# Kernel optimization log

Hardware: AMD Instinct MI355X
Metric: run time of the kernel (lower is better)

## Reference

```python
import jax, jax.numpy as jnp
import numpy as np

GROUPS = 16
EPS_GN = 1e-6
EPS_L2 = 1e-12


def setup_inputs() -> dict:
    key = jax.random.key(0)
    ks = jax.random.split(key, 5)
    B, C, H, W = 8, 256, 64, 64
    s = 0.02
    return {
        "x": jax.random.normal(ks[0], (B, C, H, W), dtype=jnp.float32),
        "gn_gamma": jnp.ones((C,), dtype=jnp.float32),
        "gn_beta": jnp.zeros((C,), dtype=jnp.float32),
        "qkv_w": jax.random.normal(ks[1], (3 * C, C), dtype=jnp.float32) * s,
        "qkv_b": jax.random.normal(ks[2], (3 * C,), dtype=jnp.float32) * s,
        "temperature": jnp.ones((1, 1, 1), dtype=jnp.float32),  # (num_heads,1,1)
        "proj_w": jax.random.normal(ks[3], (C, C), dtype=jnp.float32) * s,
        "proj_b": jax.random.normal(ks[4], (C,), dtype=jnp.float32) * s,
    }


def _group_norm(x, gamma, beta):
    B, C, H, W = x.shape
    xg = x.reshape(B, GROUPS, C // GROUPS, H, W)
    mu = xg.mean(axis=(2, 3, 4), keepdims=True)
    var = xg.var(axis=(2, 3, 4), keepdims=True)
    xn = ((xg - mu) * jax.lax.rsqrt(var + EPS_GN)).reshape(B, C, H, W)
    return xn * gamma[None, :, None, None] + beta[None, :, None, None]


def _l2norm(t):
    # normalize along last axis (token axis N), matching F.normalize eps semantics
    n = jnp.sqrt(jnp.sum(t * t, axis=-1, keepdims=True))
    return t / jnp.maximum(n, EPS_L2)


def reference(x, gn_gamma, gn_beta, qkv_w, qkv_b, temperature, proj_w, proj_b):
    B, C, H, W = x.shape
    N = H * W
    nh = 1
    dh = C // nh

    h = _group_norm(x, gn_gamma, gn_beta).reshape(B, C, N).transpose(0, 2, 1)  # (B,N,C)

    qkv = h @ qkv_w.T + qkv_b                                   # (B,N,3C)
    qkv = qkv.reshape(B, N, 3, nh, dh).transpose(2, 0, 3, 4, 1)  # (3,B,nh,dh,N)
    q, k, v = qkv[0], qkv[1], qkv[2]

    q = _l2norm(q)
    k = _l2norm(k)

    # channel cross-covariance attention: (B,nh,dh,dh)
    attn = jax.nn.softmax(jnp.einsum('bhcn,bhdn->bhcd', q, k) * temperature[None], axis=-1)
    out = jnp.einsum('bhcd,bhdn->bhcn', attn, v)                 # (B,nh,dh,N)
    out = out.transpose(0, 3, 1, 2).reshape(B, N, C)             # (B,N,C)
    out = out @ proj_w.T + proj_b

    return x + out.transpose(0, 2, 1).reshape(B, C, H, W)
```

## Files before the change

### kernel.cpp

```cpp
#include <hip/hip_runtime.h>
#include <hip/hip_bf16.h>

namespace {

constexpr float EPS_GN = 1e-6f;
constexpr float EPS_L2 = 1e-12f;

typedef __attribute__((ext_vector_type(8))) short bf16x8;
typedef __attribute__((ext_vector_type(4))) float f32x4;

__device__ __forceinline__ unsigned short f2bf(float f) {
  union { __hip_bfloat16 h; unsigned short u; } cv;
  cv.h = __float2bfloat16(f);
  return cv.u;
}
__device__ __forceinline__ float blo(unsigned u) { return __uint_as_float(u << 16); }
__device__ __forceinline__ float bhi(unsigned u) { return __uint_as_float(u & 0xffff0000u); }

__global__ __launch_bounds__(256) void prep_k(const float* __restrict__ x,
                                              const float* __restrict__ qkv_w,
                                              const float* __restrict__ proj_w,
                                              unsigned short* __restrict__ xbf,
                                              unsigned short* __restrict__ xT,
                                              float* __restrict__ sxpart,
                                              unsigned short* __restrict__ qkvw_bf,
                                              unsigned short* __restrict__ pw_bf,
                                              unsigned short* __restrict__ wvt_bf) {
  __shared__ char shm[16640];
  const int bid = blockIdx.x, t = threadIdx.x;
  if (bid < 2048) {
    unsigned short (*tl)[68] = (unsigned short (*)[68])shm;
    const int b = bid >> 8, cy = (bid >> 6) & 3, nx = bid & 63;
    const int c0 = cy * 64, n0 = nx * 64;
    const int cl = t >> 2, ns = (t & 3) * 16;
    const float* xp = x + ((size_t)b << 20) + (size_t)(c0 + cl) * 4096 + n0 + ns;
    unsigned pk[8];
    float s = 0.f;
#pragma unroll
    for (int q = 0; q < 4; ++q) {
      float4 v = *(const float4*)(xp + q * 4);
      s += v.x + v.y + v.z + v.w;
      pk[2 * q + 0] = f2bf(v.x) | ((unsigned)f2bf(v.y) << 16);
      pk[2 * q + 1] = f2bf(v.z) | ((unsigned)f2bf(v.w) << 16);
    }
    unsigned short* xo = xbf + ((size_t)b << 20) + (size_t)(c0 + cl) * 4096 + n0 + ns;
    *(int4*)xo = make_int4((int)pk[0], (int)pk[1], (int)pk[2], (int)pk[3]);
    *(int4*)(xo + 8) = make_int4((int)pk[4], (int)pk[5], (int)pk[6], (int)pk[7]);
#pragma unroll
    for (int q = 0; q < 8; ++q)
      *(unsigned*)(&tl[cl][ns + 2 * q]) = pk[q];
    s += __shfl_xor(s, 1);
    s += __shfl_xor(s, 2);
    if ((t & 3) == 0)
      sxpart[((size_t)((b * 4 + cy) * 64 + cl)) * 64 + nx] = s;
    __syncthreads();
    const int nl = t >> 2, cs2 = (t & 3) * 16;
    unsigned pk2[8];
#pragma unroll
    for (int q = 0; q < 8; ++q)
      pk2[q] = (unsigned)(unsigned short)tl[cs2 + 2 * q][nl] |
               ((unsigned)(unsigned short)tl[cs2 + 2 * q + 1][nl] << 16);
    unsigned short* to = xT + ((size_t)((b << 12) + n0 + nl)) * 256 + c0 + cs2;
    *(int4*)to = make_int4((int)pk2[0], (int)pk2[1], (int)pk2[2], (int)pk2[3]);
    *(int4*)(to + 8) = make_int4((int)pk2[4], (int)pk2[5], (int)pk2[6], (int)pk2[7]);
    return;
  }
  const int cb = bid - 2048;
  if (cb < 256) {
    const float* src = (cb < 192) ? qkv_w : proj_w;
    unsigned short* dst = (cb < 192) ? qkvw_bf : pw_bf;
    int i = (cb < 192 ? cb : cb - 192) * 256 + t;
    float4 v = ((const float4*)src)[i];
    unsigned p0 = f2bf(v.x) | ((unsigned)f2bf(v.y) << 16);
    unsigned p1 = f2bf(v.z) | ((unsigned)f2bf(v.w) << 16);
    ((int2*)dst)[i] = make_int2((int)p0, (int)p1);
    return;
  }
  float (*tlf)[65] = (float (*)[65])shm;
  const int tb = cb - 256;
  const int j0 = (tb >> 2) * 64, d0 = (tb & 3) * 64;
  const float* src = qkv_w + 512 * 256;
  const int jr = t >> 2, ds = (t & 3) * 16;
#pragma unroll
  for (int q = 0; q < 4; ++q) {
    float4 v = *(const float4*)(src + (size_t)(j0 + jr) * 256 + d0 + ds + q * 4);
    tlf[jr][ds + q * 4 + 0] = v.x; tlf[jr][ds + q * 4 + 1] = v.y;
    tlf[jr][ds + q * 4 + 2] = v.z; tlf[jr][ds + q * 4 + 3] = v.w;
  }
  __syncthreads();
  const int dr = t >> 2, js = (t & 3) * 16;
  unsigned pk[8];
#pragma unroll
  for (int q = 0; q < 8; ++q)
    pk[q] = f2bf(tlf[js + 2 * q][dr]) | ((unsigned)f2bf(tlf[js + 2 * q + 1][dr]) << 16);
  unsigned short* dp = wvt_bf + (size_t)(d0 + dr) * 256 + j0 + js;
  *(int4*)dp = make_int4((int)pk[0], (int)pk[1], (int)pk[2], (int)pk[3]);
  *(int4*)(dp + 8) = make_int4((int)pk[4], (int)pk[5], (int)pk[6], (int)pk[7]);
}

#define NT64_BODY(APTR, ALDA, BPTR, BLDB, KSTEPS)                                   \
  const int tid = threadIdx.x;                                                      \
  const int l = tid & 63, w = tid >> 6;                                             \
  const int wm = w >> 1, wn = w & 1;                                                \
  const int r = tid >> 2;                                                           \
  const unsigned short* aG = (APTR) + (size_t)(m0 + r) * (ALDA) + (tid & 3) * 16;   \
  const unsigned short* bG = (BPTR) + (size_t)(n0 + r) * (BLDB) + (tid & 3) * 16;   \
  const int g0 = (tid & 3) * 2;                                                     \
  const int w0 = r * 128 + (((g0)     ^ (r & 7)) << 4);                             \
  const int w1 = r * 128 + (((g0 + 1) ^ (r & 7)) << 4);                             \
  int rdA[2], rdB[2];                                                               \
  _Pragma("unroll")                                                                 \
  for (int i = 0; i < 2; ++i) {                                                     \
    int rm = wm * 32 + i * 16 + (l & 15);                                           \
    rdA[i] = rm * 128 + (((l >> 4) ^ (rm & 7)) << 4);                               \
    int rn = wn * 32 + i * 16 + (l & 15);                                           \
    rdB[i] = rn * 128 + (((l >> 4) ^ (rn & 7)) << 4);                               \
  }                                                                                 \
  f32x4 zero = {0.f, 0.f, 0.f, 0.f};                                                \
  f32x4 acc[2][2] = {{zero, zero}, {zero, zero}};                                   \
  for (int ks = 0; ks < (KSTEPS); ++ks) {                                           \
    int4 a0 = *(const int4*)aG, a1 = *(const int4*)(aG + 8);                        \
    int4 b0 = *(const int4*)bG, b1 = *(const int4*)(bG + 8);                        \
    aG += 64; bG += 64;                                                             \
    __syncthreads();                                                                \
    *(int4*)((char*)As + w0) = a0; *(int4*)((char*)As + w1) = a1;                   \
    *(int4*)((char*)Bs + w0) = b0; *(int4*)((char*)Bs + w1) = b1;                   \
    __syncthreads();                                                                \
    _Pragma("unroll")                                                               \
    for (int kk = 0; kk < 2; ++kk) {                                                \
      bf16x8 af[2], bf_[2];                                                         \
      _Pragma("unroll")                                                             \
      for (int i = 0; i < 2; ++i) {                                                 \
        af[i]  = *(const bf16x8*)((const char*)As + (rdA[i] ^ (kk << 6)));          \
        bf_[i] = *(const bf16x8*)((const char*)Bs + (rdB[i] ^ (kk << 6)));          \
      }                                                                             \
      _Pragma("unroll")                                                             \
      for (int i = 0; i < 2; ++i)                                                   \
        _Pragma("unroll")                                                           \
        for (int j = 0; j < 2; ++j)                                                 \
          acc[i][j] = __builtin_amdgcn_mfma_f32_16x16x32_bf16(af[i], bf_[j],        \
                                                              acc[i][j], 0, 0, 0); \
    }                                                                               \
  }                                                                                 \
  const int mB = m0 + wm * 32 + ((l >> 4) << 2);                                    \
  const int nB = n0 + wn * 32 + (l & 15);

__global__ __launch_bounds__(256) void sxx64_k(const unsigned short* __restrict__ xbf,
                                               float* __restrict__ part) {
  __shared__ unsigned short As[4096];
  __shared__ unsigned short Bs[4096];
  const int z = blockIdx.z;
  const int b = z >> 3, sl = z & 7;
  const int m0 = blockIdx.y << 6, n0 = blockIdx.x << 6;
  const unsigned short* base = xbf + ((size_t)b << 20) + (size_t)sl * 512;
  NT64_BODY(base, 4096, base, 4096, 8)
  float* po = part + ((size_t)z << 16);
#pragma unroll
  for (int i = 0; i < 2; ++i)
#pragma unroll
    for (int rr = 0; rr < 4; ++rr)
#pragma unroll
      for (int j = 0; j < 2; ++j)
        po[(size_t)(mB + i * 16 + rr) * 256 + nB + j * 16] = acc[i][j][rr];
}

__global__ __launch_bounds__(256) void out64_k(const unsigned short* __restrict__ Fbf,
                                               const unsigned short* __restrict__ xT,
                                               const float* __restrict__ hvec,
                                               float* __restrict__ outF) {
  __shared__ unsigned short As[4096];
  __shared__ unsigned short Bs[4096];
  const int b = blockIdx.z;
  const int m0 = blockIdx.y << 6, n0 = blockIdx.x << 6;
  NT64_BODY(Fbf + ((size_t)b << 16), 256, xT + ((size_t)b << 20), 256, 4)
#pragma unroll
  for (int i = 0; i < 2; ++i) {
#pragma unroll
    for (int rr = 0; rr < 4; ++rr) {
      int mi = mB + i * 16 + rr;
      float hv = hvec[b * 256 + mi];
      size_t rowo = ((size_t)b << 20) + (size_t)mi * 4096;
#pragma unroll
      for (int j = 0; j < 2; ++j)
        outF[rowo + nB + j * 16] = acc[i][j][rr] + hv;
    }
  }
}

__global__ __launch_bounds__(256) void ugemm_k(const unsigned short* __restrict__ qkvw,
                                               const unsigned short* __restrict__ Gbf,
                                               unsigned short* __restrict__ Ubf) {
  __shared__ unsigned short As[4096];
  __shared__ unsigned short Bs[4096];
  const int b = blockIdx.z;
  const int m0 = blockIdx.y << 6, n0 = blockIdx.x << 6;
  NT64_BODY(qkvw, 256, Gbf + ((size_t)b << 16), 256, 4)
  unsigned short* pu = Ubf + ((size_t)b << 17);
#pragma unroll
  for (int i = 0; i < 2; ++i)
#pragma unroll
    for (int rr = 0; rr < 4; ++rr)
#pragma unroll
      for (int j = 0; j < 2; ++j)
        pu[(size_t)(mB + i * 16 + rr) * 256 + nB + j * 16] = f2bf(acc[i][j][rr]);
}

__global__ __launch_bounds__(256) void y1h_k(const unsigned short* __restrict__ wvt,
                                             const unsigned short* __restrict__ Abf,
                                             const float* __restrict__ abv,
                                             const float* __restrict__ proj_w,
                                             const float* __restrict__ proj_b,
                                             unsigned short* __restrict__ Y1,
                                             float* __restrict__ hvec) {
  __shared__ unsigned short As[4096];
  __shared__ unsigned short Bs[4096];
  __shared__ float abl[256];
  const int b = blockIdx.z;
  const int m0 = blockIdx.y << 6, n0 = blockIdx.x << 6;
  NT64_BODY(wvt, 256, Abf + ((size_t)b << 16), 256, 4)
  unsigned short* pu = Y1 + ((size_t)b << 16);
#pragma unroll
  for (int i = 0; i < 2; ++i)
#pragma unroll
    for (int rr = 0; rr < 4; ++rr)
#pragma unroll
      for (int j = 0; j < 2; ++j)
        pu[(size_t)(mB + i * 16 + rr) * 256 + nB + j * 16] = f2bf(acc[i][j][rr]);
  if (blockIdx.y == 0) {
    abl[tid] = abv[b * 256 + tid];
    __syncthreads();
    const int t = n0 + (tid >> 2);
    const int qd = (tid & 3) * 64;
    const float* pr = proj_w + (size_t)t * 256 + qd;
    float s = 0.f;
#pragma unroll 8
    for (int i = 0; i < 64; ++i) s += pr[i] * abl[qd + i];
    s += __shfl_xor(s, 1);
    s += __shfl_xor(s, 2);
    if ((tid & 3) == 0) hvec[b * 256 + t] = proj_b[t] + s;
  }
}

__global__ __launch_bounds__(256) void fgen_k(const unsigned short* __restrict__ pw,
                                              const unsigned short* __restrict__ Y1,
                                              const float* __restrict__ avec,
                                              const float* __restrict__ evec,
                                              unsigned short* __restrict__ Fbf,
                                              float* __restrict__ hvec) {
  __shared__ unsigned short As[4096];
  __shared__ unsigned short Bs[4096];
  const int b = blockIdx.z;
  const int m0 = blockIdx.y << 6, n0 = blockIdx.x << 6;
  NT64_BODY(pw, 256, Y1 + ((size_t)b << 16), 256, 4)
  __syncthreads();
  float* hred = (float*)As;
  if (tid < 64) hred[tid] = 0.f;
  __syncthreads();
#pragma unroll
  for (int i = 0; i < 2; ++i) {
#pragma unroll
    for (int rr = 0; rr < 4; ++rr) {
      int t = mB + i * 16 + rr;
      float hp = 0.f;
#pragma unroll
      for (int j = 0; j < 2; ++j) {
        int d = nB + j * 16;
        float f = acc[i][j][rr];
        float fa = f * avec[b * 256 + d] + (t == d ? 1.f : 0.f);
        Fbf[((size_t)b << 16) + (size_t)t * 256 + d] = f2bf(fa);
        hp += f * evec[b * 256 + d];
      }
      atomicAdd(&hred[t - m0], hp);
    }
  }
  __syncthreads();
  if (tid < 64) atomicAdd(&hvec[b * 256 + m0 + tid], hred[tid]);
}

__global__ __launch_bounds__(256) void stats_k(
    const float* __restrict__ part, const float* __restrict__ sxpart,
    const float* __restrict__ gamma, const float* __restrict__ beta,
    const unsigned short* __restrict__ qkvw_bf,
    float* __restrict__ avec, float* __restrict__ evec,
    float* __restrict__ sxvec, float* __restrict__ wsv) {
  const int b = blockIdx.x, c = threadIdx.x;
  const float* sp = sxpart + ((size_t)(b * 256 + c) << 6);
  float sxv = 0.f;
#pragma unroll 4
  for (int t = 0; t < 64; ++t) sxv += sp[t];
  float dg = 0.f;
#pragma unroll
  for (int s = 0; s < 8; ++s) dg += part[((size_t)(b * 8 + s) << 16) + c * 257];
  float gs = sxv, g2 = dg;
#pragma unroll
  for (int off = 1; off < 16; off <<= 1) {
    gs += __shfl_xor(gs, off);
    g2 += __shfl_xor(g2, off);
  }
  const float inv = 1.f / 65536.f;
  float mu = gs * inv;
  float var = g2 * inv - mu * mu;
  float rstd = rsqrtf(var + EPS_GN);
  float av = gamma[c] * rstd;
  float ev = beta[c] - mu * av;
  float sv = av * sxv + 4096.f * ev;
  avec[b * 256 + c] = av; evec[b * 256 + c] = ev;
  sxvec[b * 256 + c] = sxv;
  __shared__ float sl_[256];
  sl_[c] = sv;
  __syncthreads();
  for (int i = c; i < 512; i += 256) {
    const unsigned short* wr = qkvw_bf + (size_t)i * 256;
    float acc = 0.f;
    for (int d = 0; d < 256; d += 8) {
      int4 v = *(const int4*)(wr + d);
      acc += blo((unsigned)v.x) * sl_[d + 0] + bhi((unsigned)v.x) * sl_[d + 1];
      acc += blo((unsigned)v.y) * sl_[d + 2] + bhi((unsigned)v.y) * sl_[d + 3];
      acc += blo((unsigned)v.z) * sl_[d + 4] + bhi((unsigned)v.z) * sl_[d + 5];
      acc += blo((unsigned)v.w) * sl_[d + 6] + bhi((unsigned)v.w) * sl_[d + 7];
    }
    wsv[b * 512 + i] = acc;
  }
}

__global__ __launch_bounds__(256) void gfill_k(const float* __restrict__ part,
                                               const float* __restrict__ avec,
                                               const float* __restrict__ evec,
                                               const float* __restrict__ sxvec,
                                               unsigned short* __restrict__ Gbf) {
  const int b = blockIdx.y;
  const int r = blockIdx.x * 16 + (threadIdx.x >> 4);
  const int cs = (threadIdx.x & 15) * 16;
  const float ac = avec[b * 256 + r], ec = evec[b * 256 + r], sxc = sxvec[b * 256 + r];
  unsigned pk[8];
#pragma unroll
  for (int q = 0; q < 8; ++q) {
    unsigned lohi[2];
#pragma unroll
    for (int h = 0; h < 2; ++h) {
      int d = cs + 2 * q + h;
      float S = 0.f;
#pragma unroll
      for (int s = 0; s < 8; ++s)
        S += part[(((size_t)(b * 8 + s)) << 16) + (size_t)r * 256 + d];
      float ad = avec[b * 256 + d], ed = evec[b * 256 + d], sxd = sxvec[b * 256 + d];
      float gv = ac * ad * S + ac * ed * sxc + ec * ad * sxd + 4096.f * ec * ed;
      lohi[h] = f2bf(gv);
    }
    pk[q] = lohi[0] | (lohi[1] << 16);
  }
  unsigned short* gp = Gbf + ((size_t)b << 16) + (size_t)r * 256 + cs;
  *(int4*)gp = make_int4((int)pk[0], (int)pk[1], (int)pk[2], (int)pk[3]);
  *(int4*)(gp + 8) = make_int4((int)pk[4], (int)pk[5], (int)pk[6], (int)pk[7]);
}

__global__ __launch_bounds__(256) void logsm_k(
    const unsigned short* __restrict__ Ubf,
    const unsigned short* __restrict__ qkvw,
    const float* __restrict__ wsv,
    const float* __restrict__ qkv_b, const float* __restrict__ temp,
    unsigned short* __restrict__ Abf, float* __restrict__ abv) {
  __shared__ unsigned short As[64 * 64];
  __shared__ unsigned short Bs[256 * 64];
  const int b = blockIdx.y, m0 = blockIdx.x * 64;
  const int tid = threadIdx.x;
  const int l = tid & 63, w = tid >> 6;
  const unsigned short* wk = qkvw + 65536;

  const int ar = tid >> 2, ac = tid & 3;
  const unsigned short* aG = Ubf + ((size_t)b << 17) + (size_t)(m0 + ar) * 256 + ac * 16;
  const unsigned short* bG = wk + (size_t)tid * 256;
  const int g0 = ac * 2;
  const int wA0 = ar * 128 + (((g0)     ^ (ar & 7)) << 4);
  const int wA1 = ar * 128 + (((g0 + 1) ^ (ar & 7)) << 4);
  int wBoff[8];
#pragma unroll
  for (int c = 0; c < 8; ++c) wBoff[c] = tid * 128 + ((c ^ (tid & 7)) << 4);

  int rdA;
  { int rm = w * 16 + (l & 15); rdA = rm * 128 + (((l >> 4) ^ (rm & 7)) << 4); }
  int rdB[16];
#pragma unroll
  for (int nf = 0; nf < 16; ++nf) {
    int rn = nf * 16 + (l & 15);
    rdB[nf] = rn * 128 + (((l >> 4) ^ (rn & 7)) << 4);
  }

  f32x4 zero = {0.f, 0.f, 0.f, 0.f};
  f32x4 acc[16];
#pragma unroll
  for (int nf = 0; nf < 16; ++nf) acc[nf] = zero;

  for (int ks = 0; ks < 4; ++ks) {
    int4 a0 = *(const int4*)aG;
    int4 a1 = *(const int4*)(aG + 8);
    int4 bv[8];
#pragma unroll
    for (int c = 0; c < 8; ++c) bv[c] = *(const int4*)(bG + c * 8);
    aG += 64; bG += 64;
    __syncthreads();
    *(int4*)((char*)As + wA0) = a0;
    *(int4*)((char*)As + wA1) = a1;
#pragma unroll
    for (int c = 0; c < 8; ++c) *(int4*)((char*)Bs + wBoff[c]) = bv[c];
    __syncthreads();
#pragma unroll
    for (int kk = 0; kk < 2; ++kk) {
      bf16x8 af = *(const bf16x8*)((const char*)As + (rdA ^ (kk << 6)));
#pragma unroll
      for (int nf = 0; nf < 16; ++nf) {
        bf16x8 bf_ = *(const bf16x8*)((const char*)Bs + (rdB[nf] ^ (kk << 6)));
        acc[nf] = __builtin_amdgcn_mfma_f32_16x16x32_bf16(af, bf_, acc[nf], 0, 0, 0);
      }
    }
  }

  __syncthreads();
  float* sKs  = (float*)As;
  float* sWks = sKs + 256;
  float* sBk  = sWks + 256;
  float* sBv  = sBk + 256;
  float* sQs  = sBv + 256;
  {
    const unsigned short* ur = Ubf + ((size_t)b << 17) + (size_t)(256 + tid) * 256;
    const unsigned short* wr = wk + (size_t)tid * 256;
    float dot = 0.f;
    for (int dd = 0; dd < 256; dd += 8) {
      int4 uv = *(const int4*)(ur + dd);
      int4 wv = *(const int4*)(wr + dd);
      dot += blo((unsigned)uv.x) * blo((unsigned)wv.x) + bhi((unsigned)uv.x) * bhi((unsigned)wv.x);
      dot += blo((unsigned)uv.y) * blo((unsigned)wv.y) + bhi((unsigned)uv.y) * bhi((unsigned)wv.y);
      dot += blo((unsigned)uv.z) * blo((unsigned)wv.z) + bhi((unsigned)uv.z) * bhi((unsigned)wv.z);
      dot += blo((unsigned)uv.w) * blo((unsigned)wv.w) + bhi((unsigned)uv.w) * bhi((unsigned)wv.w);
    }
    float bk = qkv_b[256 + tid];
    float wks = wsv[b * 512 + 256 + tid];
    float n2 = dot + 2.f * bk * wks + 4096.f * bk * bk;
    sKs[tid]  = 1.f / fmaxf(sqrtf(fmaxf(n2, 0.f)), EPS_L2);
    sWks[tid] = wks;
    sBk[tid]  = bk;
    sBv[tid]  = qkv_b[512 + tid];
  }
  if (tid < 64) {
    int m = m0 + tid;
    const unsigned short* ur = Ubf + ((size_t)b << 17) + (size_t)m * 256;
    const unsigned short* wr = qkvw + (size_t)m * 256;
    float dot = 0.f;
    for (int dd = 0; dd < 256; dd += 8) {
      int4 uv = *(const int4*)(ur + dd);
      int4 wv = *(const int4*)(wr + dd);
      dot += blo((unsigned)uv.x) * blo((unsigned)wv.x) + bhi((unsigned)uv.x) * bhi((unsigned)wv.x);
      dot += blo((unsigned)uv.y) * blo((unsigned)wv.y) + bhi((unsigned)uv.y) * bhi((unsigned)wv.y);
      dot += blo((unsigned)uv.z) * blo((unsigned)wv.z) + bhi((unsigned)uv.z) * bhi((unsigned)wv.z);
      dot += blo((unsigned)uv.w) * blo((unsigned)wv.w) + bhi((unsigned)uv.w) * bhi((unsigned)wv.w);
    }
    float bq = qkv_b[m], wqs = wsv[b * 512 + m];
    float n2 = dot + 2.f * bq * wqs + 4096.f * bq * bq;
    sQs[tid] = 1.f / fmaxf(sqrtf(fmaxf(n2, 0.f)), EPS_L2);
  }
  __syncthreads();

  const float T = temp[0];
  const int lrow = w * 16 + ((l >> 4) << 2);
  const int mrow = m0 + lrow;
  float ks_c[16], wks_c[16], bk_c[16], bv_c[16];
#pragma unroll
  for (int nf = 0; nf < 16; ++nf) {
    int n = nf * 16 + (l & 15);
    ks_c[nf] = sKs[n]; wks_c[nf] = sWks[n]; bk_c[nf] = sBk[n]; bv_c[nf] = sBv[n];
  }
#pragma unroll
  for (int rr = 0; rr < 4; ++rr) {
    int m = mrow + rr;
    float qs = sQs[lrow + rr], wqs = wsv[b * 512 + m], bq = qkv_b[m];
    float sc = T * qs;
#pragma unroll
    for (int nf = 0; nf < 16; ++nf)
      acc[nf][rr] = sc * ks_c[nf] *
                    (acc[nf][rr] + bq * wks_c[nf] + bk_c[nf] * wqs + 4096.f * bq * bk_c[nf]);
    float mx = acc[0][rr];
#pragma unroll
    for (int nf = 1; nf < 16; ++nf) mx = fmaxf(mx, acc[nf][rr]);
    mx = fmaxf(mx, __shfl_xor(mx, 1));
    mx = fmaxf(mx, __shfl_xor(mx, 2));
    mx = fmaxf(mx, __shfl_xor(mx, 4));
    mx = fmaxf(mx, __shfl_xor(mx, 8));
    float s = 0.f, ab = 0.f;
#pragma unroll
    for (int nf = 0; nf < 16; ++nf) {
      float e = __expf(acc[nf][rr] - mx);
      acc[nf][rr] = e;
      s += e; ab += e * bv_c[nf];
    }
#pragma unroll
    for (int off = 1; off < 16; off <<= 1) {
      s += __shfl_xor(s, off);
      ab += __shfl_xor(ab, off);
    }
    float inv = 1.f / s;
    unsigned short* arow = Abf + ((size_t)b << 16) + (size_t)m * 256 + (l & 15);
#pragma unroll
    for (int nf = 0; nf < 16; ++nf)
      arow[nf * 16] = f2bf(acc[nf][rr] * inv);
    if ((l & 15) == 0) abv[b * 256 + m] = ab * inv;
  }
}

}

extern "C" void kernel_launch(void* const* d_in, const int* in_sizes, int n_in,
                              void* d_out, int out_size, void* d_ws, size_t ws_size,
                              hipStream_t stream) {
  const float* x      = (const float*)d_in[0];
  const float* gamma  = (const float*)d_in[1];
  const float* beta   = (const float*)d_in[2];
  const float* qkv_w  = (const float*)d_in[3];
  const float* qkv_b  = (const float*)d_in[4];
  const float* temp   = (const float*)d_in[5];
  const float* proj_w = (const float*)d_in[6];
  const float* proj_b = (const float*)d_in[7];
  float* out = (float*)d_out;

  char* ws = (char*)d_ws;
  const size_t MB = 1048576;
  unsigned short* qkvw_bf = (unsigned short*)(ws);
  unsigned short* pw_bf   = (unsigned short*)(ws + 0x60000);
  unsigned short* wvt_bf  = (unsigned short*)(ws + 0x80000);
  float* avec  = (float*)(ws + 0xA0000);
  float* evec  = (float*)(ws + 0xA2000);
  float* sxvec = (float*)(ws + 0xA4000);
  float* wsv   = (float*)(ws + 0xA6000);
  float* hvec  = (float*)(ws + 0xAA000);
  float* abv   = (float*)(ws + 0xAC000);
  float* sxpart = (float*)(ws + 1 * MB);
  float* part   = (float*)(ws + 2 * MB);
  unsigned short* Gbf = (unsigned short*)(ws + 18 * MB);
  unsigned short* Ubf = (unsigned short*)(ws + 19 * MB);
  unsigned short* Abf = (unsigned short*)(ws + 21 * MB);
  unsigned short* Y1  = (unsigned short*)(ws + 22 * MB);
  unsigned short* Fbf = (unsigned short*)(ws + 23 * MB);
  unsigned short* xbf = (unsigned short*)(ws + 24 * MB);
  unsigned short* xT  = (unsigned short*)(ws + 40 * MB);
  if (ws_size < 56 * MB) return;

  prep_k<<<2320, 256, 0, stream>>>(x, qkv_w, proj_w, xbf, xT, sxpart,
                                   qkvw_bf, pw_bf, wvt_bf);

  sxx64_k<<<dim3(4, 4, 64), 256, 0, stream>>>(xbf, part);

  stats_k<<<8, 256, 0, stream>>>(part, sxpart, gamma, beta, qkvw_bf,
                                 avec, evec, sxvec, wsv);

  gfill_k<<<dim3(16, 8), 256, 0, stream>>>(part, avec, evec, sxvec, Gbf);

  ugemm_k<<<dim3(4, 8, 8), 256, 0, stream>>>(qkvw_bf, Gbf, Ubf);

  logsm_k<<<dim3(4, 8), 256, 0, stream>>>(Ubf, qkvw_bf, wsv, qkv_b, temp, Abf, abv);

  y1h_k<<<dim3(4, 4, 8), 256, 0, stream>>>(wvt_bf, Abf, abv, proj_w, proj_b, Y1, hvec);

  fgen_k<<<dim3(4, 4, 8), 256, 0, stream>>>(pw_bf, Y1, avec, evec, Fbf, hvec);

  out64_k<<<dim3(64, 4, 8), 256, 0, stream>>>(Fbf, xT, hvec, out);
}
```

Measured before the change: 115.9 us.

## Fuse six small mid-pipeline kernels into one cooperative kernel with grid syncs

Replaces the stats, gfill, ugemm, logsm, y1h and fgen launches with a single cooperative kernel of 256 blocks that runs each stage in turn, separated by grid-wide barriers. The aim is to remove the launch overhead and inter-kernel gaps between these tiny, low-occupancy stages. In exchange, most blocks sit idle in several stages, and each grid sync has its own cost. It also depends on all 256 blocks being co-resident.

```diff
diff --git a/kernel.cpp b/kernel.cpp
--- a/kernel.cpp
+++ b/kernel.cpp
@@ -1,5 +1,8 @@
 #include <hip/hip_runtime.h>
 #include <hip/hip_bf16.h>
+#include <hip/hip_cooperative_groups.h>
+
+namespace cg = cooperative_groups;
 
 namespace {
 
@@ -187,322 +190,319 @@
   }
 }
 
-__global__ __launch_bounds__(256) void ugemm_k(const unsigned short* __restrict__ qkvw,
-                                               const unsigned short* __restrict__ Gbf,
-                                               unsigned short* __restrict__ Ubf) {
-  __shared__ unsigned short As[4096];
-  __shared__ unsigned short Bs[4096];
-  const int b = blockIdx.z;
-  const int m0 = blockIdx.y << 6, n0 = blockIdx.x << 6;
-  NT64_BODY(qkvw, 256, Gbf + ((size_t)b << 16), 256, 4)
-  unsigned short* pu = Ubf + ((size_t)b << 17);
-#pragma unroll
-  for (int i = 0; i < 2; ++i)
-#pragma unroll
-    for (int rr = 0; rr < 4; ++rr)
-#pragma unroll
-      for (int j = 0; j < 2; ++j)
-        pu[(size_t)(mB + i * 16 + rr) * 256 + nB + j * 16] = f2bf(acc[i][j][rr]);
-}
-
-__global__ __launch_bounds__(256) void y1h_k(const unsigned short* __restrict__ wvt,
-                                             const unsigned short* __restrict__ Abf,
-                                             const float* __restrict__ abv,
-                                             const float* __restrict__ proj_w,
-                                             const float* __restrict__ proj_b,
-                                             unsigned short* __restrict__ Y1,
-                                             float* __restrict__ hvec) {
-  __shared__ unsigned short As[4096];
-  __shared__ unsigned short Bs[4096];
-  __shared__ float abl[256];
-  const int b = blockIdx.z;
-  const int m0 = blockIdx.y << 6, n0 = blockIdx.x << 6;
-  NT64_BODY(wvt, 256, Abf + ((size_t)b << 16), 256, 4)
-  unsigned short* pu = Y1 + ((size_t)b << 16);
-#pragma unroll
-  for (int i = 0; i < 2; ++i)
-#pragma unroll
-    for (int rr = 0; rr < 4; ++rr)
-#pragma unroll
-      for (int j = 0; j < 2; ++j)
-        pu[(size_t)(mB + i * 16 + rr) * 256 + nB + j * 16] = f2bf(acc[i][j][rr]);
-  if (blockIdx.y == 0) {
-    abl[tid] = abv[b * 256 + tid];
-    __syncthreads();
-    const int t = n0 + (tid >> 2);
-    const int qd = (tid & 3) * 64;
-    const float* pr = proj_w + (size_t)t * 256 + qd;
-    float s = 0.f;
+struct MidArgs {
+  const float* part; const float* sxpart;
+  const float* gamma; const float* beta;
+  const unsigned short* qkvw; const unsigned short* wvt; const unsigned short* pw;
+  const float* qkv_b; const float* temp;
+  const float* proj_w; const float* proj_b;
+  float* avec; float* evec; float* sxvec; float* wsv;
+  unsigned short* Gbf; unsigned short* Ubf; unsigned short* Abf;
+  unsigned short* Y1; unsigned short* Fbf;
+  float* abv; float* hvec;
+};
+
+__global__ __launch_bounds__(256) void mid_k(MidArgs p) {
+  __shared__ char shm[40960];
+  cg::grid_group gridg = cg::this_grid();
+  const int blk = blockIdx.x;
+
+  if (blk < 8) {
+    const int b = blk, c = threadIdx.x;
+    const float* sp = p.sxpart + ((size_t)(b * 256 + c) << 6);
+    float sxv = 0.f;
+#pragma unroll 4
+    for (int t = 0; t < 64; ++t) sxv += sp[t];
+    float dg = 0.f;
+#pragma unroll
+    for (int s = 0; s < 8; ++s) dg += p.part[((size_t)(b * 8 + s) << 16) + c * 257];
+    float gs = sxv, g2 = dg;
+#pragma unroll
+    for (int off = 1; off < 16; off <<= 1) {
+      gs += __shfl_xor(gs, off);
+      g2 += __shfl_xor(g2, off);
+    }
+    const float inv = 1.f / 65536.f;
+    float mu = gs * inv;
+    float var = g2 * inv - mu * mu;
+    float rstd = rsqrtf(var + EPS_GN);
+    float av = p.gamma[c] * rstd;
+    float ev = p.beta[c] - mu * av;
+    float sv = av * sxv + 4096.f * ev;
+    p.avec[b * 256 + c] = av; p.evec[b * 256 + c] = ev;
+    p.sxvec[b * 256 + c] = sxv;
+    float* sl_ = (float*)shm;
+    sl_[c] = sv;
+    __syncthreads();
+    for (int i = c; i < 512; i += 256) {
+      const unsigned short* wr = p.qkvw + (size_t)i * 256;
+      float acc = 0.f;
+      for (int d = 0; d < 256; d += 8) {
+        int4 v = *(const int4*)(wr + d);
+        acc += blo((unsigned)v.x) * sl_[d + 0] + bhi((unsigned)v.x) * sl_[d + 1];
+        acc += blo((unsigned)v.y) * sl_[d + 2] + bhi((unsigned)v.y) * sl_[d + 3];
+        acc += blo((unsigned)v.z) * sl_[d + 4] + bhi((unsigned)v.z) * sl_[d + 5];
+        acc += blo((unsigned)v.w) * sl_[d + 6] + bhi((unsigned)v.w) * sl_[d + 7];
+      }
+      p.wsv[b * 512 + i] = acc;
+    }
+  }
+  gridg.sync();
+
+  if (blk < 128) {
+    const int b = blk >> 4;
+    const int r = (blk & 15) * 16 + (threadIdx.x >> 4);
+    const int cs = (threadIdx.x & 15) * 16;
+    const float ac = p.avec[b * 256 + r], ec = p.evec[b * 256 + r], sxc = p.sxvec[b * 256 + r];
+    unsigned pk[8];
+#pragma unroll
+    for (int q = 0; q < 8; ++q) {
+      unsigned lohi[2];
+#pragma unroll
+      for (int h = 0; h < 2; ++h) {
+        int d = cs + 2 * q + h;
+        float S = 0.f;
+#pragma unroll
+        for (int s = 0; s < 8; ++s)
+          S += p.part[(((size_t)(b * 8 + s)) << 16) + (size_t)r * 256 + d];
+        float ad = p.avec[b * 256 + d], ed = p.evec[b * 256 + d], sxd = p.sxvec[b * 256 + d];
+        float gv = ac * ad * S + ac * ed * sxc + ec * ad * sxd + 4096.f * ec * ed;
+        lohi[h] = f2bf(gv);
+      }
+      pk[q] = lohi[0] | (lohi[1] << 16);
+    }
+    unsigned short* gp = p.Gbf + ((size_t)b << 16) + (size_t)r * 256 + cs;
+    *(int4*)gp = make_int4((int)pk[0], (int)pk[1], (int)pk[2], (int)pk[3]);
+    *(int4*)(gp + 8) = make_int4((int)pk[4], (int)pk[5], (int)pk[6], (int)pk[7]);
+  }
+  gridg.sync();
+
+  {
+    const int b = blk >> 5;
+    const int m0 = ((blk >> 2) & 7) << 6, n0 = (blk & 3) << 6;
+    unsigned short* As = (unsigned short*)shm;
+    unsigned short* Bs = (unsigned short*)(shm + 8192);
+    NT64_BODY(p.qkvw, 256, p.Gbf + ((size_t)b << 16), 256, 4)
+    unsigned short* pu = p.Ubf + ((size_t)b << 17);
+#pragma unroll
+    for (int i = 0; i < 2; ++i)
+#pragma unroll
+      for (int rr = 0; rr < 4; ++rr)
+#pragma unroll
+        for (int j = 0; j < 2; ++j)
+          pu[(size_t)(mB + i * 16 + rr) * 256 + nB + j * 16] = f2bf(acc[i][j][rr]);
+  }
+  gridg.sync();
+
+  if (blk < 32) {
+    const int b = blk >> 2, m0 = (blk & 3) * 64;
+    const int tid = threadIdx.x;
+    const int l = tid & 63, w = tid >> 6;
+    unsigned short* As = (unsigned short*)shm;
+    unsigned short* Bs = (unsigned short*)(shm + 8192);
+    const unsigned short* wk = p.qkvw + 65536;
+
+    const int ar = tid >> 2, ac = tid & 3;
+    const unsigned short* aG = p.Ubf + ((size_t)b << 17) + (size_t)(m0 + ar) * 256 + ac * 16;
+    const unsigned short* bG = wk + (size_t)tid * 256;
+    const int g0 = ac * 2;
+    const int wA0 = ar * 128 + (((g0)     ^ (ar & 7)) << 4);
+    const int wA1 = ar * 128 + (((g0 + 1) ^ (ar & 7)) << 4);
+    int wBoff[8];
+#pragma unroll
+    for (int c = 0; c < 8; ++c) wBoff[c] = tid * 128 + ((c ^ (tid & 7)) << 4);
+
+    int rdA;
+    { int rm = w * 16 + (l & 15); rdA = rm * 128 + (((l >> 4) ^ (rm & 7)) << 4); }
+    int rdB[16];
+#pragma unroll
+    for (int nf = 0; nf < 16; ++nf) {
+      int rn = nf * 16 + (l & 15);
+      rdB[nf] = rn * 128 + (((l >> 4) ^ (rn & 7)) << 4);
+    }
+
+    f32x4 zero = {0.f, 0.f, 0.f, 0.f};
+    f32x4 acc[16];
+#pragma unroll
+    for (int nf = 0; nf < 16; ++nf) acc[nf] = zero;
+
+    for (int ks = 0; ks < 4; ++ks) {
+      int4 a0 = *(const int4*)aG;
+      int4 a1 = *(const int4*)(aG + 8);
+      int4 bv[8];
+#pragma unroll
+      for (int c = 0; c < 8; ++c) bv[c] = *(const int4*)(bG + c * 8);
+      aG += 64; bG += 64;
+      __syncthreads();
+      *(int4*)((char*)As + wA0) = a0;
+      *(int4*)((char*)As + wA1) = a1;
+#pragma unroll
+      for (int c = 0; c < 8; ++c) *(int4*)((char*)Bs + wBoff[c]) = bv[c];
+      __syncthreads();
+#pragma unroll
+      for (int kk = 0; kk < 2; ++kk) {
+        bf16x8 af = *(const bf16x8*)((const char*)As + (rdA ^ (kk << 6)));
+#pragma unroll
+        for (int nf = 0; nf < 16; ++nf) {
+          bf16x8 bf_ = *(const bf16x8*)((const char*)Bs + (rdB[nf] ^ (kk << 6)));
+          acc[nf] = __builtin_amdgcn_mfma_f32_16x16x32_bf16(af, bf_, acc[nf], 0, 0, 0);
+        }
+      }
+    }
+
+    __syncthreads();
+    float* sKs  = (float*)As;
+    float* sWks = sKs + 256;
+    float* sBk  = sWks + 256;
+    float* sBv  = sBk + 256;
+    float* sQs  = sBv + 256;
+    {
+      const unsigned short* ur = p.Ubf + ((size_t)b << 17) + (size_t)(256 + tid) * 256;
+      const unsigned short* wr = wk + (size_t)tid * 256;
+      float dot = 0.f;
+      for (int dd = 0; dd < 256; dd += 8) {
+        int4 uv = *(const int4*)(ur + dd);
+        int4 wv = *(const int4*)(wr + dd);
+        dot += blo((unsigned)uv.x) * blo((unsigned)wv.x) + bhi((unsigned)uv.x) * bhi((unsigned)wv.x);
+        dot += blo((unsigned)uv.y) * blo((unsigned)wv.y) + bhi((unsigned)uv.y) * bhi((unsigned)wv.y);
+        dot += blo((unsigned)uv.z) * blo((unsigned)wv.z) + bhi((unsigned)uv.z) * bhi((unsigned)wv.z);
+        dot += blo((unsigned)uv.w) * blo((unsigned)wv.w) + bhi((unsigned)uv.w) * bhi((unsigned)wv.w);
+      }
+      float bk = p.qkv_b[256 + tid];
+      float wks = p.wsv[b * 512 + 256 + tid];
+      float n2 = dot + 2.f * bk * wks + 4096.f * bk * bk;
+      sKs[tid]  = 1.f / fmaxf(sqrtf(fmaxf(n2, 0.f)), EPS_L2);
+      sWks[tid] = wks;
+      sBk[tid]  = bk;
+      sBv[tid]  = p.qkv_b[512 + tid];
+    }
+    if (tid < 64) {
+      int m = m0 + tid;
+      const unsigned short* ur = p.Ubf + ((size_t)b << 17) + (size_t)m * 256;
+      const unsigned short* wr = p.qkvw + (size_t)m * 256;
+      float dot = 0.f;
+      for (int dd = 0; dd < 256; dd += 8) {
+        int4 uv = *(const int4*)(ur + dd);
+        int4 wv = *(const int4*)(wr + dd);
+        dot += blo((unsigned)uv.x) * blo((unsigned)wv.x) + bhi((unsigned)uv.x) * bhi((unsigned)wv.x);
+        dot += blo((unsigned)uv.y) * blo((unsigned)wv.y) + bhi((unsigned)uv.y) * bhi((unsigned)wv.y);
+        dot += blo((unsigned)uv.z) * blo((unsigned)wv.z) + bhi((unsigned)uv.z) * bhi((unsigned)wv.z);
+        dot += blo((unsigned)uv.w) * blo((unsigned)wv.w) + bhi((unsigned)uv.w) * bhi((unsigned)wv.w);
+      }
+      float bq = p.qkv_b[m], wqs = p.wsv[b * 512 + m];
+      float n2 = dot + 2.f * bq * wqs + 4096.f * bq * bq;
+      sQs[tid] = 1.f / fmaxf(sqrtf(fmaxf(n2, 0.f)), EPS_L2);
+    }
+    __syncthreads();
+
+    const float T = p.temp[0];
+    const int lrow = w * 16 + ((l >> 4) << 2);
+    const int mrow = m0 + lrow;
+    float ks_c[16], wks_c[16], bk_c[16], bv_c[16];
+#pragma unroll
+    for (int nf = 0; nf < 16; ++nf) {
+      int n = nf * 16 + (l & 15);
+      ks_c[nf] = sKs[n]; wks_c[nf] = sWks[n]; bk_c[nf] = sBk[n]; bv_c[nf] = sBv[n];
+    }
+#pragma unroll
+    for (int rr = 0; rr < 4; ++rr) {
+      int m = mrow + rr;
+      float qs = sQs[lrow + rr], wqs = p.wsv[b * 512 + m], bq = p.qkv_b[m];
+      float sc = T * qs;
+#pragma unroll
+      for (int nf = 0; nf < 16; ++nf)
+        acc[nf][rr] = sc * ks_c[nf] *
+                      (acc[nf][rr] + bq * wks_c[nf] + bk_c[nf] * wqs + 4096.f * bq * bk_c[nf]);
+      float mx = acc[0][rr];
+#pragma unroll
+      for (int nf = 1; nf < 16; ++nf) mx = fmaxf(mx, acc[nf][rr]);
+      mx = fmaxf(mx, __shfl_xor(mx, 1));
+      mx = fmaxf(mx, __shfl_xor(mx, 2));
+      mx = fmaxf(mx, __shfl_xor(mx, 4));
+      mx = fmaxf(mx, __shfl_xor(mx, 8));
+      float s = 0.f, ab = 0.f;
+#pragma unroll
+      for (int nf = 0; nf < 16; ++nf) {
+        float e = __expf(acc[nf][rr] - mx);
+        acc[nf][rr] = e;
+        s += e; ab += e * bv_c[nf];
+      }
+#pragma unroll
+      for (int off = 1; off < 16; off <<= 1) {
+        s += __shfl_xor(s, off);
+        ab += __shfl_xor(ab, off);
+      }
+      float inv = 1.f / s;
+      unsigned short* arow = p.Abf + ((size_t)b << 16) + (size_t)m * 256 + (l & 15);
+#pragma unroll
+      for (int nf = 0; nf < 16; ++nf)
+        arow[nf * 16] = f2bf(acc[nf][rr] * inv);
+      if ((l & 15) == 0) p.abv[b * 256 + m] = ab * inv;
+    }
+  }
+  gridg.sync();
+
+  if (blk < 128) {
+    const int b = blk >> 4;
+    const int by = (blk >> 2) & 3;
+    const int m0 = by << 6, n0 = (blk & 3) << 6;
+    unsigned short* As = (unsigned short*)shm;
+    unsigned short* Bs = (unsigned short*)(shm + 8192);
+    float* abl = (float*)(shm + 16384);
+    NT64_BODY(p.wvt, 256, p.Abf + ((size_t)b << 16), 256, 4)
+    unsigned short* pu = p.Y1 + ((size_t)b << 16);
+#pragma unroll
+    for (int i = 0; i < 2; ++i)
+#pragma unroll
+      for (int rr = 0; rr < 4; ++rr)
+#pragma unroll
+        for (int j = 0; j < 2; ++j)
+          pu[(size_t)(mB + i * 16 + rr) * 256 + nB + j * 16] = f2bf(acc[i][j][rr]);
+    if (by == 0) {
+      abl[tid] = p.abv[b * 256 + tid];
+      __syncthreads();
+      const int t = n0 + (tid >> 2);
+      const int qd = (tid & 3) * 64;
+      const float* pr = p.proj_w + (size_t)t * 256 + qd;
+      float s = 0.f;
 #pragma unroll 8
-    for (int i = 0; i < 64; ++i) s += pr[i] * abl[qd + i];
-    s += __shfl_xor(s, 1);
-    s += __shfl_xor(s, 2);
-    if ((tid & 3) == 0) hvec[b * 256 + t] = proj_b[t] + s;
-  }
-}
-
-__global__ __launch_bounds__(256) void fgen_k(const unsigned short* __restrict__ pw,
-                                              const unsigned short* __restrict__ Y1,
-                                              const float* __restrict__ avec,
-                                              const float* __restrict__ evec,
-                                              unsigned short* __restrict__ Fbf,
-                                              float* __restrict__ hvec) {
-  __shared__ unsigned short As[4096];
-  __shared__ unsigned short Bs[4096];
-  const int b = blockIdx.z;
-  const int m0 = blockIdx.y << 6, n0 = blockIdx.x << 6;
-  NT64_BODY(pw, 256, Y1 + ((size_t)b << 16), 256, 4)
-  __syncthreads();
-  float* hred = (float*)As;
-  if (tid < 64) hred[tid] = 0.f;
-  __syncthreads();
-#pragma unroll
-  for (int i = 0; i < 2; ++i) {
-#pragma unroll
-    for (int rr = 0; rr < 4; ++rr) {
-      int t = mB + i * 16 + rr;
-      float hp = 0.f;
-#pragma unroll
-      for (int j = 0; j < 2; ++j) {
-        int d = nB + j * 16;
-        float f = acc[i][j][rr];
-        float fa = f * avec[b * 256 + d] + (t == d ? 1.f : 0.f);
-        Fbf[((size_t)b << 16) + (size_t)t * 256 + d] = f2bf(fa);
-        hp += f * evec[b * 256 + d];
-      }
-      atomicAdd(&hred[t - m0], hp);
-    }
-  }
-  __syncthreads();
-  if (tid < 64) atomicAdd(&hvec[b * 256 + m0 + tid], hred[tid]);
-}
-
-__global__ __launch_bounds__(256) void stats_k(
-    const float* __restrict__ part, const float* __restrict__ sxpart,
-    const float* __restrict__ gamma, const float* __restrict__ beta,
-    const unsigned short* __restrict__ qkvw_bf,
-    float* __restrict__ avec, float* __restrict__ evec,
-    float* __restrict__ sxvec, float* __restrict__ wsv) {
-  const int b = blockIdx.x, c = threadIdx.x;
-  const float* sp = sxpart + ((size_t)(b * 256 + c) << 6);
-  float sxv = 0.f;
-#pragma unroll 4
-  for (int t = 0; t < 64; ++t) sxv += sp[t];
-  float dg = 0.f;
-#pragma unroll
-  for (int s = 0; s < 8; ++s) dg += part[((size_t)(b * 8 + s) << 16) + c * 257];
-  float gs = sxv, g2 = dg;
-#pragma unroll
-  for (int off = 1; off < 16; off <<= 1) {
-    gs += __shfl_xor(gs, off);
-    g2 += __shfl_xor(g2, off);
-  }
-  const float inv = 1.f / 65536.f;
-  float mu = gs * inv;
-  float var = g2 * inv - mu * mu;
-  float rstd = rsqrtf(var + EPS_GN);
-  float av = gamma[c] * rstd;
-  float ev = beta[c] - mu * av;
-  float sv = av * sxv + 4096.f * ev;
-  avec[b * 256 + c] = av; evec[b * 256 + c] = ev;
-  sxvec[b * 256 + c] = sxv;
-  __shared__ float sl_[256];
-  sl_[c] = sv;
-  __syncthreads();
-  for (int i = c; i < 512; i += 256) {
-    const unsigned short* wr = qkvw_bf + (size_t)i * 256;
-    float acc = 0.f;
-    for (int d = 0; d < 256; d += 8) {
-      int4 v = *(const int4*)(wr + d);
-      acc += blo((unsigned)v.x) * sl_[d + 0] + bhi((unsigned)v.x) * sl_[d + 1];
-      acc += blo((unsigned)v.y) * sl_[d + 2] + bhi((unsigned)v.y) * sl_[d + 3];
-      acc += blo((unsigned)v.z) * sl_[d + 4] + bhi((unsigned)v.z) * sl_[d + 5];
-      acc += blo((unsigned)v.w) * sl_[d + 6] + bhi((unsigned)v.w) * sl_[d + 7];
-    }
-    wsv[b * 512 + i] = acc;
-  }
-}
-
-__global__ __launch_bounds__(256) void gfill_k(const float* __restrict__ part,
-                                               const float* __restrict__ avec,
-                                               const float* __restrict__ evec,
-                                               const float* __restrict__ sxvec,
-                                               unsigned short* __restrict__ Gbf) {
-  const int b = blockIdx.y;
-  const int r = blockIdx.x * 16 + (threadIdx.x >> 4);
-  const int cs = (threadIdx.x & 15) * 16;
-  const float ac = avec[b * 256 + r], ec = evec[b * 256 + r], sxc = sxvec[b * 256 + r];
-  unsigned pk[8];
-#pragma unroll
-  for (int q = 0; q < 8; ++q) {
-    unsigned lohi[2];
-#pragma unroll
-    for (int h = 0; h < 2; ++h) {
-      int d = cs + 2 * q + h;
-      float S = 0.f;
-#pragma unroll
-      for (int s = 0; s < 8; ++s)
-        S += part[(((size_t)(b * 8 + s)) << 16) + (size_t)r * 256 + d];
-      float ad = avec[b * 256 + d], ed = evec[b * 256 + d], sxd = sxvec[b * 256 + d];
-      float gv = ac * ad * S + ac * ed * sxc + ec * ad * sxd + 4096.f * ec * ed;
-      lohi[h] = f2bf(gv);
-    }
-    pk[q] = lohi[0] | (lohi[1] << 16);
-  }
-  unsigned short* gp = Gbf + ((size_t)b << 16) + (size_t)r * 256 + cs;
-  *(int4*)gp = make_int4((int)pk[0], (int)pk[1], (int)pk[2], (int)pk[3]);
-  *(int4*)(gp + 8) = make_int4((int)pk[4], (int)pk[5], (int)pk[6], (int)pk[7]);
-}
-
-__global__ __launch_bounds__(256) void logsm_k(
-    const unsigned short* __restrict__ Ubf,
-    const unsigned short* __restrict__ qkvw,
-    const float* __restrict__ wsv,
-    const float* __restrict__ qkv_b, const float* __restrict__ temp,
-    unsigned short* __restrict__ Abf, float* __restrict__ abv) {
-  __shared__ unsigned short As[64 * 64];
-  __shared__ unsigned short Bs[256 * 64];
-  const int b = blockIdx.y, m0 = blockIdx.x * 64;
-  const int tid = threadIdx.x;
-  const int l = tid & 63, w = tid >> 6;
-  const unsigned short* wk = qkvw + 65536;
-
-  const int ar = tid >> 2, ac = tid & 3;
-  const unsigned short* aG = Ubf + ((size_t)b << 17) + (size_t)(m0 + ar) * 256 + ac * 16;
-  const unsigned short* bG = wk + (size_t)tid * 256;
-  const int g0 = ac * 2;
-  const int wA0 = ar * 128 + (((g0)     ^ (ar & 7)) << 4);
-  const int wA1 = ar * 128 + (((g0 + 1) ^ (ar & 7)) << 4);
-  int wBoff[8];
-#pragma unroll
-  for (int c = 0; c < 8; ++c) wBoff[c] = tid * 128 + ((c ^ (tid & 7)) << 4);
-
-  int rdA;
-  { int rm = w * 16 + (l & 15); rdA = rm * 128 + (((l >> 4) ^ (rm & 7)) << 4); }
-  int rdB[16];
-#pragma unroll
-  for (int nf = 0; nf < 16; ++nf) {
-    int rn = nf * 16 + (l & 15);
-    rdB[nf] = rn * 128 + (((l >> 4) ^ (rn & 7)) << 4);
-  }
-
-  f32x4 zero = {0.f, 0.f, 0.f, 0.f};
-  f32x4 acc[16];
-#pragma unroll
-  for (int nf = 0; nf < 16; ++nf) acc[nf] = zero;
-
-  for (int ks = 0; ks < 4; ++ks) {
-    int4 a0 = *(const int4*)aG;
-    int4 a1 = *(const int4*)(aG + 8);
-    int4 bv[8];
-#pragma unroll
-    for (int c = 0; c < 8; ++c) bv[c] = *(const int4*)(bG + c * 8);
-    aG += 64; bG += 64;
-    __syncthreads();
-    *(int4*)((char*)As + wA0) = a0;
-    *(int4*)((char*)As + wA1) = a1;
-#pragma unroll
-    for (int c = 0; c < 8; ++c) *(int4*)((char*)Bs + wBoff[c]) = bv[c];
-    __syncthreads();
-#pragma unroll
-    for (int kk = 0; kk < 2; ++kk) {
-      bf16x8 af = *(const bf16x8*)((const char*)As + (rdA ^ (kk << 6)));
-#pragma unroll
-      for (int nf = 0; nf < 16; ++nf) {
-        bf16x8 bf_ = *(const bf16x8*)((const char*)Bs + (rdB[nf] ^ (kk << 6)));
-        acc[nf] = __builtin_amdgcn_mfma_f32_16x16x32_bf16(af, bf_, acc[nf], 0, 0, 0);
-      }
-    }
-  }
-
-  __syncthreads();
-  float* sKs  = (float*)As;
-  float* sWks = sKs + 256;
-  float* sBk  = sWks + 256;
-  float* sBv  = sBk + 256;
-  float* sQs  = sBv + 256;
-  {
-    const unsigned short* ur = Ubf + ((size_t)b << 17) + (size_t)(256 + tid) * 256;
-    const unsigned short* wr = wk + (size_t)tid * 256;
-    float dot = 0.f;
-    for (int dd = 0; dd < 256; dd += 8) {
-      int4 uv = *(const int4*)(ur + dd);
-      int4 wv = *(const int4*)(wr + dd);
-      dot += blo((unsigned)uv.x) * blo((unsigned)wv.x) + bhi((unsigned)uv.x) * bhi((unsigned)wv.x);
-      dot += blo((unsigned)uv.y) * blo((unsigned)wv.y) + bhi((unsigned)uv.y) * bhi((unsigned)wv.y);
-      dot += blo((unsigned)uv.z) * blo((unsigned)wv.z) + bhi((unsigned)uv.z) * bhi((unsigned)wv.z);
-      dot += blo((unsigned)uv.w) * blo((unsigned)wv.w) + bhi((unsigned)uv.w) * bhi((unsigned)wv.w);
-    }
-    float bk = qkv_b[256 + tid];
-    float wks = wsv[b * 512 + 256 + tid];
-    float n2 = dot + 2.f * bk * wks + 4096.f * bk * bk;
-    sKs[tid]  = 1.f / fmaxf(sqrtf(fmaxf(n2, 0.f)), EPS_L2);
-    sWks[tid] = wks;
-    sBk[tid]  = bk;
-    sBv[tid]  = qkv_b[512 + tid];
-  }
-  if (tid < 64) {
-    int m = m0 + tid;
-    const unsigned short* ur = Ubf + ((size_t)b << 17) + (size_t)m * 256;
-    const unsigned short* wr = qkvw + (size_t)m * 256;
-    float dot = 0.f;
-    for (int dd = 0; dd < 256; dd += 8) {
-      int4 uv = *(const int4*)(ur + dd);
-      int4 wv = *(const int4*)(wr + dd);
-      dot += blo((unsigned)uv.x) * blo((unsigned)wv.x) + bhi((unsigned)uv.x) * bhi((unsigned)wv.x);
-      dot += blo((unsigned)uv.y) * blo((unsigned)wv.y) + bhi((unsigned)uv.y) * bhi((unsigned)wv.y);
-      dot += blo((unsigned)uv.z) * blo((unsigned)wv.z) + bhi((unsigned)uv.z) * bhi((unsigned)wv.z);
-      dot += blo((unsigned)uv.w) * blo((unsigned)wv.w) + bhi((unsigned)uv.w) * bhi((unsigned)wv.w);
-    }
-    float bq = qkv_b[m], wqs = wsv[b * 512 + m];
-    float n2 = dot + 2.f * bq * wqs + 4096.f * bq * bq;
-    sQs[tid] = 1.f / fmaxf(sqrtf(fmaxf(n2, 0.f)), EPS_L2);
-  }
-  __syncthreads();
-
-  const float T = temp[0];
-  const int lrow = w * 16 + ((l >> 4) << 2);
-  const int mrow = m0 + lrow;
-  float ks_c[16], wks_c[16], bk_c[16], bv_c[16];
-#pragma unroll
-  for (int nf = 0; nf < 16; ++nf) {
-    int n = nf * 16 + (l & 15);
-    ks_c[nf] = sKs[n]; wks_c[nf] = sWks[n]; bk_c[nf] = sBk[n]; bv_c[nf] = sBv[n];
-  }
-#pragma unroll
-  for (int rr = 0; rr < 4; ++rr) {
-    int m = mrow + rr;
-    float qs = sQs[lrow + rr], wqs = wsv[b * 512 + m], bq = qkv_b[m];
-    float sc = T * qs;
-#pragma unroll
-    for (int nf = 0; nf < 16; ++nf)
-      acc[nf][rr] = sc * ks_c[nf] *
-                    (acc[nf][rr] + bq * wks_c[nf] + bk_c[nf] * wqs + 4096.f * bq * bk_c[nf]);
-    float mx = acc[0][rr];
-#pragma unroll
-    for (int nf = 1; nf < 16; ++nf) mx = fmaxf(mx, acc[nf][rr]);
-    mx = fmaxf(mx, __shfl_xor(mx, 1));
-    mx = fmaxf(mx, __shfl_xor(mx, 2));
-    mx = fmaxf(mx, __shfl_xor(mx, 4));
-    mx = fmaxf(mx, __shfl_xor(mx, 8));
-    float s = 0.f, ab = 0.f;
-#pragma unroll
-    for (int nf = 0; nf < 16; ++nf) {
-      float e = __expf(acc[nf][rr] - mx);
-      acc[nf][rr] = e;
-      s += e; ab += e * bv_c[nf];
-    }
-#pragma unroll
-    for (int off = 1; off < 16; off <<= 1) {
-      s += __shfl_xor(s, off);
-      ab += __shfl_xor(ab, off);
-    }
-    float inv = 1.f / s;
-    unsigned short* arow = Abf + ((size_t)b << 16) + (size_t)m * 256 + (l & 15);
-#pragma unroll
-    for (int nf = 0; nf < 16; ++nf)
-      arow[nf * 16] = f2bf(acc[nf][rr] * inv);
-    if ((l & 15) == 0) abv[b * 256 + m] = ab * inv;
+      for (int i = 0; i < 64; ++i) s += pr[i] * abl[qd + i];
+      s += __shfl_xor(s, 1);
+      s += __shfl_xor(s, 2);
+      if ((tid & 3) == 0) p.hvec[b * 256 + t] = p.proj_b[t] + s;
+    }
+  }
+  gridg.sync();
+
+  if (blk < 128) {
+    const int b = blk >> 4;
+    const int m0 = ((blk >> 2) & 3) << 6, n0 = (blk & 3) << 6;
+    unsigned short* As = (unsigned short*)shm;
+    unsigned short* Bs = (unsigned short*)(shm + 8192);
+    NT64_BODY(p.pw, 256, p.Y1 + ((size_t)b << 16), 256, 4)
+    __syncthreads();
+    float* hred = (float*)As;
+    if (tid < 64) hred[tid] = 0.f;
+    __syncthreads();
+#pragma unroll
+    for (int i = 0; i < 2; ++i) {
+#pragma unroll
+      for (int rr = 0; rr < 4; ++rr) {
+        int t = mB + i * 16 + rr;
+        float hp = 0.f;
+#pragma unroll
+        for (int j = 0; j < 2; ++j) {
+          int d = nB + j * 16;
+          float f = acc[i][j][rr];
+          float fa = f * p.avec[b * 256 + d] + (t == d ? 1.f : 0.f);
+          p.Fbf[((size_t)b << 16) + (size_t)t * 256 + d] = f2bf(fa);
+          hp += f * p.evec[b * 256 + d];
+        }
+        atomicAdd(&hred[t - m0], hp);
+      }
+    }
+    __syncthreads();
+    if (tid < 64) atomicAdd(&p.hvec[b * 256 + m0 + tid], hred[tid]);
   }
 }
 
@@ -548,18 +548,18 @@
 
   sxx64_k<<<dim3(4, 4, 64), 256, 0, stream>>>(xbf, part);
 
-  stats_k<<<8, 256, 0, stream>>>(part, sxpart, gamma, beta, qkvw_bf,
-                                 avec, evec, sxvec, wsv);
-
-  gfill_k<<<dim3(16, 8), 256, 0, stream>>>(part, avec, evec, sxvec, Gbf);
-
-  ugemm_k<<<dim3(4, 8, 8), 256, 0, stream>>>(qkvw_bf, Gbf, Ubf);
-
-  logsm_k<<<dim3(4, 8), 256, 0, stream>>>(Ubf, qkvw_bf, wsv, qkv_b, temp, Abf, abv);
-
-  y1h_k<<<dim3(4, 4, 8), 256, 0, stream>>>(wvt_bf, Abf, abv, proj_w, proj_b, Y1, hvec);
-
-  fgen_k<<<dim3(4, 4, 8), 256, 0, stream>>>(pw_bf, Y1, avec, evec, Fbf, hvec);
+  MidArgs margs;
+  margs.part = part; margs.sxpart = sxpart;
+  margs.gamma = gamma; margs.beta = beta;
+  margs.qkvw = qkvw_bf; margs.wvt = wvt_bf; margs.pw = pw_bf;
+  margs.qkv_b = qkv_b; margs.temp = temp;
+  margs.proj_w = proj_w; margs.proj_b = proj_b;
+  margs.avec = avec; margs.evec = evec; margs.sxvec = sxvec; margs.wsv = wsv;
+  margs.Gbf = Gbf; margs.Ubf = Ubf; margs.Abf = Abf;
+  margs.Y1 = Y1; margs.Fbf = Fbf;
+  margs.abv = abv; margs.hvec = hvec;
+  void* kp[] = {(void*)&margs};
+  hipLaunchCooperativeKernel((const void*)mid_k, dim3(256), dim3(256), kp, 0, stream);
 
   out64_k<<<dim3(64, 4, 8), 256, 0, stream>>>(Fbf, xT, hvec, out);
 }
```

Measured after the change: 253.9 us. 2.19x slower.
